# Optimization experiments

Measured on AMD Instinct MI355X. Metric: run time of the kernel, lower is better.

## Reference

```python
import jax, jax.numpy as jnp
import numpy as np

P, N, A = 8, 160, 32            # poses, blocks per pose, atoms per block (tile size)
BT = 24                         # number of block types
MAX_DON, MAX_ACC = 4, 8         # max donor-H / acceptor slots per block tile
ND, NAT = 16, 16                # donor / acceptor chemical types
NPAIR = ND * NAT                # donor-type x acceptor-type pair table size
NPOLY = 11                      # degree-10 polynomial: 11 coefficients
MIN_SEP = 4                     # minimum bond separation for an hbond


def setup_inputs() -> dict:
    key = jax.random.key(0)
    ks = jax.random.split(key, 12)
    coords = jax.random.normal(ks[0], (P, N * A, 3), jnp.float32) * 10.0
    # dispatch every ordered block pair in every pose: (pose, block1, block2)
    pp, bb1, bb2 = jnp.meshgrid(jnp.arange(P), jnp.arange(N), jnp.arange(N), indexing="ij")
    block_pair_dispatch_indices = jnp.stack(
        [pp.ravel(), bb1.ravel(), bb2.ravel()], axis=-1
    ).astype(jnp.int32)
    pose_stack_block_coord_offset = jnp.tile(
        (jnp.arange(N, dtype=jnp.int32) * A)[None, :], (P, 1)
    )
    pose_stack_block_type = jax.random.randint(ks[1], (P, N), 0, BT, jnp.int32)
    pose_stack_min_bond_separation = jax.random.randint(ks[2], (P, N, N), 0, 6, jnp.int32)
    bt_tile_n_donH = jax.random.randint(ks[3], (BT,), 0, MAX_DON + 1, jnp.int32)
    bt_tile_n_acc = jax.random.randint(ks[4], (BT,), 0, MAX_ACC + 1, jnp.int32)
    bt_tile_donH_inds = jax.random.randint(ks[5], (BT, MAX_DON), 0, A, jnp.int32)
    bt_tile_acc_inds = jax.random.randint(ks[6], (BT, MAX_ACC), 0, A, jnp.int32)
    bt_tile_donor_type = jax.random.randint(ks[7], (BT, MAX_DON), 0, ND, jnp.int32)
    bt_tile_acceptor_type = jax.random.randint(ks[8], (BT, MAX_ACC), 0, NAT, jnp.int32)
    bt_tile_acceptor_hybridization = jax.random.randint(ks[9], (BT, MAX_ACC), 0, 3, jnp.int32)
    pair_params = jax.random.uniform(ks[10], (NPAIR, 3), jnp.float32, 0.5, 1.5)
    pair_polynomials = jax.random.normal(ks[11], (NPAIR, NPOLY), jnp.float32) * 0.01
    # [max_AH_distance, min_energy_clamp, unused, unused]
    global_params = jnp.array([6.0, -2.0, 0.0, 1.0], jnp.float32)
    return dict(
        coords=coords,
        block_pair_dispatch_indices=block_pair_dispatch_indices,
        pose_stack_block_coord_offset=pose_stack_block_coord_offset,
        pose_stack_block_type=pose_stack_block_type,
        pose_stack_min_bond_separation=pose_stack_min_bond_separation,
        bt_tile_n_donH=bt_tile_n_donH,
        bt_tile_n_acc=bt_tile_n_acc,
        bt_tile_donH_inds=bt_tile_donH_inds,
        bt_tile_acc_inds=bt_tile_acc_inds,
        bt_tile_donor_type=bt_tile_donor_type,
        bt_tile_acceptor_type=bt_tile_acceptor_type,
        bt_tile_acceptor_hybridization=bt_tile_acceptor_hybridization,
        pair_params=pair_params,
        pair_polynomials=pair_polynomials,
        global_params=global_params,
    )


def reference(coords, block_pair_dispatch_indices, pose_stack_block_coord_offset,
              pose_stack_block_type, pose_stack_min_bond_separation,
              bt_tile_n_donH, bt_tile_n_acc, bt_tile_donH_inds, bt_tile_acc_inds,
              bt_tile_donor_type, bt_tile_acceptor_type,
              bt_tile_acceptor_hybridization, pair_params, pair_polynomials,
              global_params):
    p = block_pair_dispatch_indices[:, 0]   # [K]
    b1 = block_pair_dispatch_indices[:, 1]
    b2 = block_pair_dispatch_indices[:, 2]
    bt1 = pose_stack_block_type[p, b1]      # [K] block type of donor block
    bt2 = pose_stack_block_type[p, b2]      # [K] block type of acceptor block
    off1 = pose_stack_block_coord_offset[p, b1]
    off2 = pose_stack_block_coord_offset[p, b2]

    don_atoms = bt_tile_donH_inds[bt1]      # [K, MD] donor-H atom slots
    acc_atoms = bt_tile_acc_inds[bt2]       # [K, MA] acceptor atom slots
    H = coords[p[:, None], off1[:, None] + don_atoms]   # [K, MD, 3]
    Ac = coords[p[:, None], off2[:, None] + acc_atoms]  # [K, MA, 3]

    # AH distances for every donor-H x acceptor candidate in the pair
    diff = H[:, :, None, :] - Ac[:, None, :, :]          # [K, MD, MA, 3]
    d = jnp.sqrt(jnp.sum(diff * diff, axis=-1) + 1e-12)  # [K, MD, MA]

    # pair-type index into the donor_type x acceptor_type tables
    pt = bt_tile_donor_type[bt1][:, :, None] * NAT + bt_tile_acceptor_type[bt2][:, None, :]

    # Horner evaluation of the degree-10 AH-distance polynomial; gather one
    # coefficient column per step to avoid a [K, MD, MA, 11] intermediate.
    e = pair_polynomials[pt, 0]
    for c in range(1, NPOLY):
        e = e * d + pair_polynomials[pt, c]

    # hybridization-dependent weight (sp2 / sp3 / ring)
    hyb = jnp.broadcast_to(bt_tile_acceptor_hybridization[bt2][:, None, :], pt.shape)
    w = pair_params[pt, hyb]                              # [K, MD, MA]

    # validity: slot within donor/acceptor counts, distinct blocks,
    # sufficient bond separation, within distance cutoff
    don_valid = jnp.arange(MAX_DON)[None, :] < bt_tile_n_donH[bt1][:, None]
    acc_valid = jnp.arange(MAX_ACC)[None, :] < bt_tile_n_acc[bt2][:, None]
    pair_ok = (b1 != b2) & (pose_stack_min_bond_separation[p, b1, b2] >= MIN_SEP)
    valid = (don_valid[:, :, None] & acc_valid[:, None, :]
             & pair_ok[:, None, None] & (d < global_params[0]))

    e = jnp.maximum(jnp.minimum(e, 0.0), global_params[1])  # clamp to [min_E, 0]
    energy = jnp.where(valid, w * e, 0.0)                    # [K, MD, MA]

    # scatter-accumulate per-pair energies into per-pose totals
    pose_energies = jax.ops.segment_sum(
        jnp.sum(energy, axis=(1, 2)), p, num_segments=P)     # [P]
    return pose_energies
```

## Files before the change

### kernel.cpp

```cpp
#include <hip/hip_runtime.h>

#define NP 8
#define NB 160
#define NA 32
#define NATYPE 16
#define NPOLY 11
#define MIN_SEP 4
#define DVALID (1 << 16)
#define NWG (NP * NB)
#define MAGICU 0x48424F4Eu

__global__ __launch_bounds__(256) void hbond_kernel(
    const float* __restrict__ coords,
    const int*   __restrict__ coord_off,
    const int*   __restrict__ block_type,
    const int*   __restrict__ min_sep,
    const int*   __restrict__ n_donH,
    const int*   __restrict__ n_acc,
    const int*   __restrict__ donH_inds,
    const int*   __restrict__ acc_inds,
    const int*   __restrict__ donor_type,
    const int*   __restrict__ acceptor_type,
    const int*   __restrict__ acceptor_hyb,
    const float* __restrict__ pair_params,
    const float* __restrict__ pair_poly,
    const float* __restrict__ gp,
    unsigned long long* __restrict__ slots,
    float*       __restrict__ out)
{
    const int t  = threadIdx.x;
    const int p  = blockIdx.x / NB;
    const int b1 = blockIdx.x - p * NB;

    __shared__ int4  b2info[NB];
    __shared__ int   b2list[NB];
    __shared__ int   wc[4];
    __shared__ float wsum[4];

    const float cut  = gp[0];
    const float emin = gp[1];

    bool ok = false;
    if (t < NB) {
        const int bt2  = block_type[p * NB + t];
        const int off2 = coord_off[p * NB + t];
        const int na   = n_acc[bt2];
        ok = (t != b1) && (min_sep[(p * NB + b1) * NB + t] >= MIN_SEP);
        b2info[t] = make_int4(bt2, off2, na, 0);
    }

    const int bt1  = block_type[p * NB + b1];
    const int off1 = coord_off[p * NB + b1];
    const int nd   = n_donH[bt1];
    float4 dv[4];
    #pragma unroll
    for (int dn = 0; dn < 4; ++dn) {
        const int hatom = donH_inds[bt1 * 4 + dn];
        const int dbase = donor_type[bt1 * 4 + dn] * NATYPE;
        const float* Hc = coords + (size_t)(p * (NB * NA) + off1 + hatom) * 3;
        dv[dn] = make_float4(Hc[0], Hc[1], Hc[2],
                             __int_as_float((dbase & 0xff) | ((dn < nd) ? DVALID : 0)));
    }

    const unsigned long long m = __ballot(ok);
    const int wv = t >> 6, ln = t & 63;
    if (ln == 0) wc[wv] = __popcll(m);
    __syncthreads();

    int pre = 0, cnt = 0;
    #pragma unroll
    for (int w = 0; w < 4; ++w) {
        cnt += wc[w];
        if (w < wv) pre += wc[w];
    }
    if (ok) b2list[pre + __popcll(m & ((1ull << ln) - 1ull))] = t;
    __syncthreads();

    float energy = 0.0f;
    const int cnt8 = cnt * 8;
    for (int i = t; i < cnt8; i += 256) {
        const int b2 = b2list[i >> 3];
        const int a  = i & 7;
        const int4 info = b2info[b2];

        float hd0 = 0, hd1 = 0, hd2 = 0, hd3 = 0;
        int   hp0 = 0, hp1 = 0, hp2 = 0, hp3 = 0;
        int   nh = 0, hyb = 0;

        if (a < info.z) {
            const int ai    = acc_inds[info.x * 8 + a];
            const int atype = acceptor_type[info.x * 8 + a];
            hyb             = acceptor_hyb[info.x * 8 + a];
            const float* Ac = coords + (size_t)(p * (NB * NA) + info.y + ai) * 3;
            const float ax = Ac[0], ay = Ac[1], az = Ac[2];

            #pragma unroll
            for (int dn = 0; dn < 4; ++dn) {
                const int dbits = __float_as_int(dv[dn].w);
                if (!(dbits & DVALID)) continue;
                const float dx = dv[dn].x - ax;
                const float dy = dv[dn].y - ay;
                const float dz = dv[dn].z - az;
                const float dd = sqrtf(dx * dx + dy * dy + dz * dz + 1e-12f);
                if (dd < cut) {
                    const int pp = (dbits & 0xff) + atype;
                    hd3 = (nh == 3) ? dd : hd3;  hp3 = (nh == 3) ? pp : hp3;
                    hd2 = (nh == 2) ? dd : hd2;  hp2 = (nh == 2) ? pp : hp2;
                    hd1 = (nh == 1) ? dd : hd1;  hp1 = (nh == 1) ? pp : hp1;
                    hd0 = (nh == 0) ? dd : hd0;  hp0 = (nh == 0) ? pp : hp0;
                    ++nh;
                }
            }
        }

        #pragma unroll
        for (int h = 0; h < 4; ++h) {
            if (!__any(h < nh)) break;
            if (h < nh) {
                const float dd = (h == 0) ? hd0 : (h == 1) ? hd1 : (h == 2) ? hd2 : hd3;
                const int   pp = (h == 0) ? hp0 : (h == 1) ? hp1 : (h == 2) ? hp2 : hp3;
                const float* c = pair_poly + pp * NPOLY;
                float ev = c[0];
                #pragma unroll
                for (int k = 1; k < NPOLY; ++k) ev = ev * dd + c[k];
                const float w = pair_params[pp * 3 + hyb];
                ev = fmaxf(fminf(ev, 0.0f), emin);
                energy += w * ev;
            }
        }
    }

    #pragma unroll
    for (int off = 32; off >= 1; off >>= 1)
        energy += __shfl_down(energy, off, 64);
    if (ln == 0) wsum[wv] = energy;
    __syncthreads();
    if (t == 0) {
        const float s = wsum[0] + wsum[1] + wsum[2] + wsum[3];
        const unsigned long long v =
            ((unsigned long long)MAGICU << 32) |
            (unsigned long long)(unsigned int)__float_as_int(s);
        __hip_atomic_store(&slots[blockIdx.x], v,
                           __ATOMIC_RELAXED, __HIP_MEMORY_SCOPE_AGENT);
    }

    if (blockIdx.x == 0) {
        #pragma unroll
        for (int q = 0; q < 2; ++q) {
            const int pose = wv * 2 + q;
            unsigned long long* base = slots + pose * NB;
            float acc = 0.0f;
            #pragma unroll
            for (int r = 0; r < 3; ++r) {
                const int idx = r * 64 + ln;
                if (idx < NB) {
                    unsigned long long v;
                    for (;;) {
                        v = __hip_atomic_load(&base[idx], __ATOMIC_RELAXED,
                                              __HIP_MEMORY_SCOPE_AGENT);
                        if ((unsigned int)(v >> 32) == MAGICU) break;
                        __builtin_amdgcn_s_sleep(1);
                    }
                    acc += __int_as_float((int)(unsigned int)(v & 0xffffffffull));
                    __hip_atomic_store(&base[idx], 0ull,
                                       __ATOMIC_RELAXED, __HIP_MEMORY_SCOPE_AGENT);
                }
            }
            #pragma unroll
            for (int off = 32; off >= 1; off >>= 1)
                acc += __shfl_down(acc, off, 64);
            if (ln == 0) out[pose] = acc;
        }
    }
}

extern "C" void kernel_launch(void* const* d_in, const int* in_sizes, int n_in,
                              void* d_out, int out_size, void* d_ws, size_t ws_size,
                              hipStream_t stream) {
    const float* coords        = (const float*)d_in[0];
    const int*   coord_off     = (const int*)  d_in[2];
    const int*   block_type    = (const int*)  d_in[3];
    const int*   min_sep       = (const int*)  d_in[4];
    const int*   n_donH        = (const int*)  d_in[5];
    const int*   n_acc         = (const int*)  d_in[6];
    const int*   donH_inds     = (const int*)  d_in[7];
    const int*   acc_inds      = (const int*)  d_in[8];
    const int*   donor_type    = (const int*)  d_in[9];
    const int*   acceptor_type = (const int*)  d_in[10];
    const int*   acceptor_hyb  = (const int*)  d_in[11];
    const float* pair_params   = (const float*)d_in[12];
    const float* pair_poly     = (const float*)d_in[13];
    const float* gp            = (const float*)d_in[14];
    unsigned long long* slots  = (unsigned long long*)d_ws;
    float*       out           = (float*)d_out;

    hbond_kernel<<<NWG, 256, 0, stream>>>(
        coords, coord_off, block_type, min_sep,
        n_donH, n_acc, donH_inds, acc_inds,
        donor_type, acceptor_type, acceptor_hyb,
        pair_params, pair_poly, gp, slots, out);
}
```

Before: 12.96 us.

## Move final reduction to dedicated per-pose consumer blocks and drop block-level sum

Result: no change. 12.89 us (-0.5%).

```diff
diff --git a/kernel.cpp b/kernel.cpp
--- a/kernel.cpp
+++ b/kernel.cpp
@@ -7,7 +7,8 @@
 #define NPOLY 11
 #define MIN_SEP 4
 #define DVALID (1 << 16)
-#define NWG (NP * NB)
+#define NPROD (NP * NB)
+#define SLOTS_PER_POSE (NB * 4)
 #define MAGICU 0x48424F4Eu
 
 __global__ __launch_bounds__(256) void hbond_kernel(
@@ -29,13 +30,42 @@
     float*       __restrict__ out)
 {
     const int t  = threadIdx.x;
+    const int wv = t >> 6, ln = t & 63;
+
+    if (blockIdx.x >= NPROD) {
+        const int pose = blockIdx.x - NPROD;
+        unsigned long long* base = slots + pose * SLOTS_PER_POSE;
+        __shared__ float rsum[4];
+
+        float acc = 0.0f;
+        for (int idx = t; idx < SLOTS_PER_POSE; idx += 256) {
+            unsigned long long v;
+            for (;;) {
+                v = __hip_atomic_load(&base[idx], __ATOMIC_RELAXED,
+                                      __HIP_MEMORY_SCOPE_AGENT);
+                if ((unsigned int)(v >> 32) == MAGICU) break;
+                __builtin_amdgcn_s_sleep(1);
+            }
+            acc += __int_as_float((int)(unsigned int)(v & 0xffffffffull));
+        }
+        #pragma unroll
+        for (int off = 32; off >= 1; off >>= 1)
+            acc += __shfl_down(acc, off, 64);
+        if (ln == 0) rsum[wv] = acc;
+        __syncthreads();
+        if (t == 0) out[pose] = rsum[0] + rsum[1] + rsum[2] + rsum[3];
+        for (int idx = t; idx < SLOTS_PER_POSE; idx += 256)
+            __hip_atomic_store(&base[idx], 0ull,
+                               __ATOMIC_RELAXED, __HIP_MEMORY_SCOPE_AGENT);
+        return;
+    }
+
     const int p  = blockIdx.x / NB;
     const int b1 = blockIdx.x - p * NB;
 
-    __shared__ int4  b2info[NB];
-    __shared__ int   b2list[NB];
-    __shared__ int   wc[4];
-    __shared__ float wsum[4];
+    __shared__ int4 b2info[NB];
+    __shared__ int  b2list[NB];
+    __shared__ int  wc[4];
 
     const float cut  = gp[0];
     const float emin = gp[1];
@@ -63,7 +93,6 @@
     }
 
     const unsigned long long m = __ballot(ok);
-    const int wv = t >> 6, ln = t & 63;
     if (ln == 0) wc[wv] = __popcll(m);
     __syncthreads();
 
@@ -122,7 +151,7 @@
                 const float* c = pair_poly + pp * NPOLY;
                 float ev = c[0];
                 #pragma unroll
-                for (int k = 1; k < NPOLY; ++k) ev = ev * dd + c[k];
+                for (int kk = 1; kk < NPOLY; ++kk) ev = ev * dd + c[kk];
                 const float w = pair_params[pp * 3 + hyb];
                 ev = fmaxf(fminf(ev, 0.0f), emin);
                 energy += w * ev;
@@ -133,44 +162,12 @@
     #pragma unroll
     for (int off = 32; off >= 1; off >>= 1)
         energy += __shfl_down(energy, off, 64);
-    if (ln == 0) wsum[wv] = energy;
-    __syncthreads();
-    if (t == 0) {
-        const float s = wsum[0] + wsum[1] + wsum[2] + wsum[3];
+    if (ln == 0) {
         const unsigned long long v =
             ((unsigned long long)MAGICU << 32) |
-            (unsigned long long)(unsigned int)__float_as_int(s);
-        __hip_atomic_store(&slots[blockIdx.x], v,
+            (unsigned long long)(unsigned int)__float_as_int(energy);
+        __hip_atomic_store(&slots[(p * NB + b1) * 4 + wv], v,
                            __ATOMIC_RELAXED, __HIP_MEMORY_SCOPE_AGENT);
-    }
-
-    if (blockIdx.x == 0) {
-        #pragma unroll
-        for (int q = 0; q < 2; ++q) {
-            const int pose = wv * 2 + q;
-            unsigned long long* base = slots + pose * NB;
-            float acc = 0.0f;
-            #pragma unroll
-            for (int r = 0; r < 3; ++r) {
-                const int idx = r * 64 + ln;
-                if (idx < NB) {
-                    unsigned long long v;
-                    for (;;) {
-                        v = __hip_atomic_load(&base[idx], __ATOMIC_RELAXED,
-                                              __HIP_MEMORY_SCOPE_AGENT);
-                        if ((unsigned int)(v >> 32) == MAGICU) break;
-                        __builtin_amdgcn_s_sleep(1);
-                    }
-                    acc += __int_as_float((int)(unsigned int)(v & 0xffffffffull));
-                    __hip_atomic_store(&base[idx], 0ull,
-                                       __ATOMIC_RELAXED, __HIP_MEMORY_SCOPE_AGENT);
-                }
-            }
-            #pragma unroll
-            for (int off = 32; off >= 1; off >>= 1)
-                acc += __shfl_down(acc, off, 64);
-            if (ln == 0) out[pose] = acc;
-        }
     }
 }
 
@@ -194,7 +191,7 @@
     unsigned long long* slots  = (unsigned long long*)d_ws;
     float*       out           = (float*)d_out;
 
-    hbond_kernel<<<NWG, 256, 0, stream>>>(
+    hbond_kernel<<<NPROD + NP, 256, 0, stream>>>(
         coords, coord_off, block_type, min_sep,
         n_donH, n_acc, donH_inds, acc_inds,
         donor_type, acceptor_type, acceptor_hyb,
```
